# Kernel tuning notes

Hardware: AMD Instinct MI355X
Metric: run time of the kernel (lower is better)

The kernel has to match this reference:

```python
import jax, jax.numpy as jnp
import numpy as np

D_MODEL = 512
N_HEADS = 16
D_HEAD = D_MODEL // N_HEADS


def _relative_shift(pos_score):
    # pos_score: [B, H, T, T]  (Transformer-XL shift trick)
    B, H, T1, T2 = pos_score.shape
    padded = jnp.pad(pos_score, ((0, 0), (0, 0), (0, 0), (1, 0)))  # [B,H,T1,T2+1]
    padded = padded.reshape(B, H, T2 + 1, T1)
    return padded[:, :, 1:].reshape(B, H, T1, T2)


def setup_inputs() -> dict:
    key = jax.random.key(0)
    ks = jax.random.split(key, 12)
    B, T, D = 4, 1024, D_MODEL
    s = 1.0 / np.sqrt(D)
    return {
        "q": jax.random.normal(ks[0], (B, T, D), jnp.float32),
        "k": jax.random.normal(ks[1], (B, T, D), jnp.float32),
        "v": jax.random.normal(ks[2], (B, T, D), jnp.float32),
        "pos_embedding": jax.random.normal(ks[3], (B, T, D), jnp.float32),
        "Wq": jax.random.normal(ks[4], (D, D), jnp.float32) * s,
        "bq": jnp.zeros((D,), jnp.float32),
        "Wp": jax.random.normal(ks[5], (D, D), jnp.float32) * s,
        "Wf": jax.random.normal(ks[6], (D, D), jnp.float32) * s,
        "bf": jnp.zeros((D,), jnp.float32),
        "u_bias": jax.random.normal(ks[7], (N_HEADS, D_HEAD), jnp.float32) * s,
        "v_bias": jax.random.normal(ks[8], (N_HEADS, D_HEAD), jnp.float32) * s,
    }


def reference(q, k, v, pos_embedding, Wq, bq, Wp, Wf, bf, u_bias, v_bias):
    B, T, D = q.shape
    H, Dh = N_HEADS, D_HEAD
    sqrt_dim = jnp.asarray(np.sqrt(D_MODEL), q.dtype)
    # NOTE: original module uses linear_q for q, k AND v (faithful to source)
    qh = (q @ Wq + bq).reshape(B, T, H, Dh)            # [B,T,H,Dh]
    kh = (k @ Wq + bq).reshape(B, T, H, Dh)
    vh = (v @ Wq + bq).reshape(B, T, H, Dh)
    ph = (pos_embedding @ Wp).reshape(B, T, H, Dh)     # no bias

    content_score = jnp.einsum('bthd,bshd->bhts', qh + u_bias, kh)
    pos_score = jnp.einsum('bthd,bshd->bhts', qh + v_bias, ph)
    pos_score = _relative_shift(pos_score)

    score = (content_score + pos_score) / sqrt_dim     # [B,H,T,T]
    attn = jax.nn.softmax(score, axis=-1)              # dropout identity in eval
    context = jnp.einsum('bhts,bshd->bthd', attn, vh).reshape(B, T, D)
    return context @ Wf + bf
```

## Files before the change

### kernel.cpp

```cpp
#include <hip/hip_runtime.h>
#include <hip/hip_bf16.h>

typedef __bf16 bf16;
typedef bf16 bf16x8 __attribute__((ext_vector_type(8)));
typedef bf16 bf16x4 __attribute__((ext_vector_type(4)));
typedef float f32x4 __attribute__((ext_vector_type(4)));
typedef _Float16 f16x4 __attribute__((ext_vector_type(4)));

#define SCALE_LOG2 0.06376237f


__global__ __launch_bounds__(256) void prep_kernel(
    const float* __restrict__ Wq, const float* __restrict__ Wp, const float* __restrict__ Wf,
    bf16* __restrict__ WqT, bf16* __restrict__ WpT, bf16* __restrict__ WfT)
{
  const int tid = threadIdx.x;
  __shared__ bf16 t[64][72];
  const int m = blockIdx.x >> 6;
  const int tb = blockIdx.x & 63;
  const int tr = tb >> 3, tc = tb & 7;
  const float* W = (m == 0) ? Wq : (m == 1) ? Wp : Wf;
  bf16*        O = (m == 0) ? WqT : (m == 1) ? WpT : WfT;
  const int r = tid >> 2, cg = tid & 3;
  {
    const float* src = W + (size_t)(tr * 64 + r) * 512 + tc * 64 + cg * 16;
    f32x4 a = *(const f32x4*)src, b2 = *(const f32x4*)(src + 4);
    f32x4 c = *(const f32x4*)(src + 8), d = *(const f32x4*)(src + 12);
    bf16x8 lo, hi;
#pragma unroll
    for (int j = 0; j < 4; j++) { lo[j] = (bf16)a[j]; lo[4 + j] = (bf16)b2[j]; hi[j] = (bf16)c[j]; hi[4 + j] = (bf16)d[j]; }
    *(bf16x8*)(&t[r][cg * 16])     = lo;
    *(bf16x8*)(&t[r][cg * 16 + 8]) = hi;
  }
  __syncthreads();
  bf16x8 o0, o1;
#pragma unroll
  for (int j = 0; j < 8; j++) { o0[j] = t[cg * 16 + j][r]; o1[j] = t[cg * 16 + 8 + j][r]; }
  bf16* dst = O + (size_t)(tc * 64 + r) * 512 + tr * 64 + cg * 16;
  *(bf16x8*)dst = o0;
  *(bf16x8*)(dst + 8) = o1;
}

__global__ __launch_bounds__(256) void proj_gemm(
    const float* __restrict__ q, const float* __restrict__ k, const float* __restrict__ v,
    const float* __restrict__ pos,
    const bf16* __restrict__ WqT, const bf16* __restrict__ WpT, const float* __restrict__ bq,
    bf16* __restrict__ qh, bf16* __restrict__ kh, bf16* __restrict__ vT, bf16* __restrict__ phx)
{
  __shared__ bf16 ABs[2 * 128 * 72];
  bf16* As = ABs;
  bf16* Bs = ABs + 128 * 72;
  bf16* vtile = ABs;
  const int tid = threadIdx.x;
  const int wave = tid >> 6, lane = tid & 63, quad = lane >> 4, ln = lane & 15;
  const int wg = blockIdx.x;
  const int xcd = wg & 7, sidx = wg >> 3;
  const int tn = sidx & 3;
  const int tm = xcd + ((sidx >> 2) << 3);
  const int kind = tm >> 5;
  const int rr0 = (tm & 31) * 128;
  const float* X = (kind == 0) ? q : (kind == 1) ? k : (kind == 2) ? v : pos;
  const bf16* WT = ((kind < 3) ? WqT : WpT) + (size_t)tn * 128 * 512;
  const int qn_ = (wave & 1) * 64;
  const int qr_ = (wave >> 1) * 64;
  const int srow = tid >> 2, scg = tid & 3;

  f32x4 acc[4][4] = {};

  f32x4  xa0[4], xa1[4];
  bf16x8 wr0[2], wr1[2];
  {
    const float* p0 = X + (size_t)(rr0 + srow) * 512 + scg * 16;
    const float* p1 = X + (size_t)(rr0 + srow + 64) * 512 + scg * 16;
#pragma unroll
    for (int u = 0; u < 4; u++) { xa0[u] = *(const f32x4*)(p0 + u * 4); xa1[u] = *(const f32x4*)(p1 + u * 4); }
    const bf16* w0 = WT + (size_t)srow * 512 + scg * 16;
    const bf16* w1 = WT + (size_t)(srow + 64) * 512 + scg * 16;
    wr0[0] = *(const bf16x8*)w0; wr0[1] = *(const bf16x8*)(w0 + 8);
    wr1[0] = *(const bf16x8*)w1; wr1[1] = *(const bf16x8*)(w1 + 8);
  }

  for (int kk = 0; kk < 8; kk++) {
    __syncthreads();
    {
      bf16x8 lo, hi;
#pragma unroll
      for (int j = 0; j < 4; j++) { lo[j] = (bf16)xa0[0][j]; lo[4 + j] = (bf16)xa0[1][j]; hi[j] = (bf16)xa0[2][j]; hi[4 + j] = (bf16)xa0[3][j]; }
      *(bf16x8*)(As + srow * 72 + scg * 16)     = lo;
      *(bf16x8*)(As + srow * 72 + scg * 16 + 8) = hi;
#pragma unroll
      for (int j = 0; j < 4; j++) { lo[j] = (bf16)xa1[0][j]; lo[4 + j] = (bf16)xa1[1][j]; hi[j] = (bf16)xa1[2][j]; hi[4 + j] = (bf16)xa1[3][j]; }
      *(bf16x8*)(As + (srow + 64) * 72 + scg * 16)     = lo;
      *(bf16x8*)(As + (srow + 64) * 72 + scg * 16 + 8) = hi;
      *(bf16x8*)(Bs + srow * 72 + scg * 16)            = wr0[0];
      *(bf16x8*)(Bs + srow * 72 + scg * 16 + 8)        = wr0[1];
      *(bf16x8*)(Bs + (srow + 64) * 72 + scg * 16)     = wr1[0];
      *(bf16x8*)(Bs + (srow + 64) * 72 + scg * 16 + 8) = wr1[1];
    }
    __syncthreads();

    if (kk < 7) {
      const int k0n = (kk + 1) * 64;
      const float* p0 = X + (size_t)(rr0 + srow) * 512 + k0n + scg * 16;
      const float* p1 = X + (size_t)(rr0 + srow + 64) * 512 + k0n + scg * 16;
#pragma unroll
      for (int u = 0; u < 4; u++) { xa0[u] = *(const f32x4*)(p0 + u * 4); xa1[u] = *(const f32x4*)(p1 + u * 4); }
      const bf16* w0 = WT + (size_t)srow * 512 + k0n + scg * 16;
      const bf16* w1 = WT + (size_t)(srow + 64) * 512 + k0n + scg * 16;
      wr0[0] = *(const bf16x8*)w0; wr0[1] = *(const bf16x8*)(w0 + 8);
      wr1[0] = *(const bf16x8*)w1; wr1[1] = *(const bf16x8*)(w1 + 8);
    }

#pragma unroll
    for (int ks = 0; ks < 2; ks++) {
      bf16x8 wf[4], xf[4];
#pragma unroll
      for (int i = 0; i < 4; i++) {
        wf[i] = *(const bf16x8*)(Bs + (qn_ + i * 16 + ln) * 72 + ks * 32 + quad * 8);
        xf[i] = *(const bf16x8*)(As + (qr_ + i * 16 + ln) * 72 + ks * 32 + quad * 8);
      }
#pragma unroll
      for (int i = 0; i < 4; i++)
#pragma unroll
        for (int j = 0; j < 4; j++)
          acc[i][j] = __builtin_amdgcn_mfma_f32_16x16x32_bf16(wf[i], xf[j], acc[i][j], 0, 0, 0);
    }
  }
  __syncthreads();

  if (kind == 2) {
#pragma unroll
    for (int i = 0; i < 4; i++) {
      const int nloc = qn_ + i * 16 + quad * 4;
      f32x4 b4 = *(const f32x4*)(bq + tn * 128 + nloc);
#pragma unroll
      for (int j = 0; j < 4; j++) {
        const int mloc = qr_ + j * 16 + ln;
        bf16x4 pk;
#pragma unroll
        for (int r = 0; r < 4; r++) pk[r] = (bf16)(acc[i][j][r] + b4[r]);
        *(bf16x4*)(vtile + mloc * 132 + nloc) = pk;
      }
    }
    __syncthreads();
    const int n = tid >> 1, mh = (tid & 1) * 64;
    const int bb2 = rr0 >> 10, tt0 = rr0 & 1023;
    bf16* vdst = vT + ((size_t)(bb2 * 16 + tn * 4 + (n >> 5)) * 32 + (n & 31)) * 1024 + tt0 + mh;
#pragma unroll
    for (int c = 0; c < 8; c++) {
      bf16x8 oc;
#pragma unroll
      for (int e = 0; e < 8; e++) oc[e] = vtile[(mh + c * 8 + e) * 132 + n];
      *(bf16x8*)(vdst + c * 8) = oc;
    }
  } else {
#pragma unroll
    for (int i = 0; i < 4; i++) {
      const int nn0 = tn * 128 + qn_ + i * 16 + quad * 4;
      const int dd0 = nn0 & 31, hh = nn0 >> 5;
      f32x4 b4 = {0.f, 0.f, 0.f, 0.f};
      if (kind < 3) b4 = *(const f32x4*)(bq + nn0);
#pragma unroll
      for (int j = 0; j < 4; j++) {
        const int rr = rr0 + qr_ + j * 16 + ln;
        const int bb = rr >> 10, tt = rr & 1023;
        const size_t base = (size_t)(bb * 16 + hh);
        bf16x4 pk;
#pragma unroll
        for (int r = 0; r < 4; r++) pk[r] = (bf16)(acc[i][j][r] + b4[r]);
        if (kind == 0)      *(bf16x4*)(qh + (base * 1024 + tt) * 32 + dd0) = pk;
        else if (kind == 1) *(bf16x4*)(kh + (base * 1024 + tt) * 32 + dd0) = pk;
        else {
          *(bf16x4*)(phx + (base * 2048 + tt) * 32 + dd0) = pk;
          if (tt <= 1021) *(bf16x4*)(phx + (base * 2048 + tt + 1025) * 32 + dd0) = pk;
          if (tt == 1023) {
            bf16x4 zz = {};
            *(bf16x4*)(phx + (base * 2048 + 1024) * 32 + dd0) = zz;
            *(bf16x4*)(phx + (base * 2048 + 2047) * 32 + dd0) = zz;
          }
        }
      }
    }
  }
}

__global__ __launch_bounds__(256, 4) void attn_kernel(
    const bf16* __restrict__ qh, const bf16* __restrict__ kh,
    const bf16* __restrict__ vT, const bf16* __restrict__ phx,
    const float* __restrict__ u_bias, const float* __restrict__ v_bias,
    float* __restrict__ Oa, float* __restrict__ Ob,
    float* __restrict__ la, float* __restrict__ lb)
{
  __shared__ bf16     kst[2][64 * 40];
  __shared__ bf16     phs[2][128 * 40];
  __shared__ bf16     vst[2][32 * 72];
  __shared__ _Float16 fs[4 * 16 * 84];
  __shared__ bf16     pb[4 * 16 * 72];

  const int tid = threadIdx.x;
  const int wave = tid >> 6, lane = tid & 63, quad = lane >> 4, ln = lane & 15;
  const int wg = blockIdx.x;
  const int bh = wg & 63;
  const int rest = wg >> 6;
  const int tq = rest & 15, sc = rest >> 4;
  const int h = bh & 15, b = bh >> 4;
  const int t0 = tq * 64;
  const bf16* qh_h  = qh  + (size_t)bh * 1024 * 32;
  const bf16* kh_h  = kh  + (size_t)bh * 1024 * 32;
  const bf16* vT_h  = vT  + (size_t)bh * 32 * 1024;
  const bf16* phx_h = phx + (size_t)bh * 2048 * 32;

  _Float16* fsw = fs + wave * 16 * 84;
  bf16*     pbw = pb + wave * 16 * 72;

  const int sr4 = tid >> 2, sc4 = tid & 3;
  const int sr8 = tid >> 3, sc8 = tid & 7;

  const int Ab  = quad * 4 + ((15 - ln) & ~3);
  const int msh = ((15 - ln) & 3) * 16;

  bf16x8 qu, qva, qvn;
  {
    const int t = t0 + wave * 16 + ln;
    bf16x8 q0 = *(const bf16x8*)(qh_h + (size_t)t * 32 + quad * 8);
    bf16x8 q1 = *(const bf16x8*)(qh_h + (size_t)(t + 1) * 32 + quad * 8);
    const float* ubp = u_bias + h * 32 + quad * 8;
    const float* vbp = v_bias + h * 32 + quad * 8;
#pragma unroll
    for (int j = 0; j < 8; j++) {
      qu[j]  = (bf16)(((float)q0[j] + ubp[j]) * SCALE_LOG2);
      qva[j] = (bf16)(((float)q0[j] + vbp[j]) * SCALE_LOG2);
      qvn[j] = (bf16)(((float)q1[j] + vbp[j]) * SCALE_LOG2);
    }
  }

  f32x4 O0 = {0.f, 0.f, 0.f, 0.f}, O1 = {0.f, 0.f, 0.f, 0.f};
  float l_lane = 0.0f;
  const f32x4 zf = {0.f, 0.f, 0.f, 0.f};

  const int si0 = sc * 8;

  bf16x8 g0, g1, g2, g3;
  {
    const int s0p = si0 * 64, jbp = s0p - t0 + 960;
    g0 = *(const bf16x8*)(kh_h  + (size_t)(s0p + sr4) * 32 + sc4 * 8);
    g1 = *(const bf16x8*)(phx_h + (size_t)(jbp + sr4) * 32 + sc4 * 8);
    g2 = *(const bf16x8*)(phx_h + (size_t)(jbp + 64 + sr4) * 32 + sc4 * 8);
    g3 = *(const bf16x8*)(vT_h  + (size_t)sr8 * 1024 + s0p + sc8 * 8);
  }

#pragma unroll 2
  for (int si = si0; si < si0 + 8; si++) {
    const int buf = si & 1;
    const int s0 = si * 64;
    const int jbase = s0 - t0 + 960;
    const int jb0 = jbase + (3 - wave) * 16;
    bf16* kc = kst[buf];
    bf16* pc = phs[buf];
    bf16* vc = vst[buf];

    *(bf16x8*)(kc + sr4 * 40 + sc4 * 8)        = g0;
    *(bf16x8*)(pc + sr4 * 40 + sc4 * 8)        = g1;
    *(bf16x8*)(pc + (64 + sr4) * 40 + sc4 * 8) = g2;
    *(bf16x8*)(vc + sr8 * 72 + sc8 * 8)        = g3;

    __syncthreads();

    if (si != si0 + 7) {
      const int s0n = s0 + 64, jbn = jbase + 64;
      g0 = *(const bf16x8*)(kh_h  + (size_t)(s0n + sr4) * 32 + sc4 * 8);
      g1 = *(const bf16x8*)(phx_h + (size_t)(jbn + sr4) * 32 + sc4 * 8);
      g2 = *(const bf16x8*)(phx_h + (size_t)(jbn + 64 + sr4) * 32 + sc4 * 8);
      g3 = *(const bf16x8*)(vT_h  + (size_t)sr8 * 1024 + s0n + sc8 * 8);
    }

#pragma unroll
    for (int i = 0; i < 5; i++) {
      const int row = (3 - wave + i) * 16 + ln;
      bf16x8 pbf = *(const bf16x8*)(pc + row * 40 + quad * 8);
      bf16x8 bsel = (jb0 + i * 16 >= 1024) ? qvn : qva;
      f32x4 f = __builtin_amdgcn_mfma_f32_16x16x32_bf16(pbf, bsel, zf, 0, 0, 0);
      f16x4 fh;
#pragma unroll
      for (int r = 0; r < 4; r++) fh[r] = (_Float16)f[r];
      *(f16x4*)(fsw + ln * 84 + i * 16 + quad * 4) = fh;
    }

    f32x4 c[4];
#pragma unroll
    for (int cs = 0; cs < 4; cs++) {
      bf16x8 kbf = *(const bf16x8*)(kc + (cs * 16 + ln) * 40 + quad * 8);
      c[cs] = __builtin_amdgcn_mfma_f32_16x16x32_bf16(kbf, qu, zf, 0, 0, 0);
    }

    const _Float16* rowp = fsw + ln * 84;
#pragma unroll
    for (int cs = 0; cs < 4; cs++) {
      const uint64_t v0 = *(const uint64_t*)(rowp + cs * 16 + Ab);
      const uint64_t v1 = *(const uint64_t*)(rowp + cs * 16 + Ab + 4);
      union { uint64_t u; f16x4 v; } W;
      W.u = (v0 >> msh) | ((v1 << 1) << (63 - msh));
      bf16x4 pk;
#pragma unroll
      for (int r = 0; r < 4; r++) {
        const float p = __builtin_amdgcn_exp2f(c[cs][r] + (float)W.v[r]);
        l_lane += p;
        pk[r] = (bf16)p;
      }
      *(bf16x4*)(pbw + ln * 72 + cs * 16 + quad * 4) = pk;
    }

#pragma unroll
    for (int kb = 0; kb < 2; kb++) {
      bf16x8 a  = *(const bf16x8*)(pbw + ln * 72 + kb * 32 + quad * 8);
      bf16x8 b0 = *(const bf16x8*)(vc + ln * 72 + kb * 32 + quad * 8);
      bf16x8 b1 = *(const bf16x8*)(vc + (16 + ln) * 72 + kb * 32 + quad * 8);
      O0 = __builtin_amdgcn_mfma_f32_16x16x32_bf16(a, b0, O0, 0, 0, 0);
      O1 = __builtin_amdgcn_mfma_f32_16x16x32_bf16(a, b1, O1, 0, 0, 0);
    }
  }

  l_lane += __shfl_xor(l_lane, 16);
  l_lane += __shfl_xor(l_lane, 32);

  float* Op = sc ? Ob : Oa;
  float* lp = sc ? lb : la;
#pragma unroll
  for (int r = 0; r < 4; r++) {
    const int t = t0 + wave * 16 + quad * 4 + r;
    const size_t o = ((size_t)(b * 1024 + t)) * 512 + h * 32;
    Op[o + ln]      = O0[r];
    Op[o + 16 + ln] = O1[r];
  }
  if (lane < 16) lp[(size_t)bh * 1024 + t0 + wave * 16 + lane] = l_lane;
}

__global__ __launch_bounds__(256) void out_gemm(
    const float* __restrict__ Oa, const float* __restrict__ Ob,
    const float* __restrict__ la, const float* __restrict__ lb,
    const bf16* __restrict__ WfT, const float* __restrict__ bfv,
    float* __restrict__ out)
{
  __shared__ bf16 As[32 * 40];
  __shared__ bf16 Bs[128 * 40];
  __shared__ float linv[16 * 32];
  const int tid = threadIdx.x;
  const int wave = tid >> 6, lane = tid & 63, quad = lane >> 4, ln = lane & 15;
  const int wg = blockIdx.x;
  const int xcd = wg & 7, sidx = wg >> 3;
  const int tn = sidx & 3;
  const int tm = xcd + ((sidx >> 2) << 3);
  const int rr0 = tm * 32;
  const bf16* WT = WfT + (size_t)tn * 128 * 512;
  const int qm = (wave & 1) * 16, qn = (wave >> 1) * 64;
  const int srow = tid >> 2, scg = tid & 3;
  const int srow8 = tid >> 3, scg8 = tid & 7;

  f32x4 a0, c0;
  bf16x8 b0r, b1r;
  {
    a0 = *(const f32x4*)(Oa + (size_t)(rr0 + srow8) * 512 + scg8 * 4);
    c0 = *(const f32x4*)(Ob + (size_t)(rr0 + srow8) * 512 + scg8 * 4);
    b0r = *(const bf16x8*)(WT + (size_t)srow * 512 + scg * 8);
    b1r = *(const bf16x8*)(WT + (size_t)(srow + 64) * 512 + scg * 8);
  }

  for (int e = tid; e < 512; e += 256) {
    const int hh = e >> 5, r = e & 31;
    const int row = rr0 + r;
    const int b_ = row >> 10, t_ = row & 1023;
    const size_t li = ((size_t)(b_ * 16 + hh)) * 1024 + t_;
    linv[e] = 1.0f / (la[li] + lb[li]);
  }

  f32x4 acc[4] = {};
  for (int kk = 0; kk < 16; kk++) {
    __syncthreads();
    {
      const float s = linv[kk * 32 + srow8];
      bf16x4 t4;
#pragma unroll
      for (int j = 0; j < 4; j++) t4[j] = (bf16)((a0[j] + c0[j]) * s);
      *(bf16x4*)(As + srow8 * 40 + scg8 * 4)      = t4;
      *(bf16x8*)(Bs + srow * 40 + scg * 8)        = b0r;
      *(bf16x8*)(Bs + (srow + 64) * 40 + scg * 8) = b1r;
    }
    __syncthreads();

    if (kk < 15) {
      const int k0n = (kk + 1) * 32;
      a0 = *(const f32x4*)(Oa + (size_t)(rr0 + srow8) * 512 + k0n + scg8 * 4);
      c0 = *(const f32x4*)(Ob + (size_t)(rr0 + srow8) * 512 + k0n + scg8 * 4);
      b0r = *(const bf16x8*)(WT + (size_t)srow * 512 + k0n + scg * 8);
      b1r = *(const bf16x8*)(WT + (size_t)(srow + 64) * 512 + k0n + scg * 8);
    }

    bf16x8 af, bfm[4];
    af = *(const bf16x8*)(As + (qm + ln) * 40 + quad * 8);
#pragma unroll
    for (int j = 0; j < 4; j++)
      bfm[j] = *(const bf16x8*)(Bs + (qn + j * 16 + ln) * 40 + quad * 8);
#pragma unroll
    for (int j = 0; j < 4; j++)
      acc[j] = __builtin_amdgcn_mfma_f32_16x16x32_bf16(af, bfm[j], acc[j], 0, 0, 0);
  }

#pragma unroll
  for (int j = 0; j < 4; j++) {
    const int nn = tn * 128 + qn + j * 16 + ln;
    const float bias = bfv[nn];
#pragma unroll
    for (int r = 0; r < 4; r++) {
      const int rr = rr0 + qm + quad * 4 + r;
      out[(size_t)rr * 512 + nn] = acc[j][r] + bias;
    }
  }
}

extern "C" void kernel_launch(void* const* d_in, const int* in_sizes, int n_in,
                              void* d_out, int out_size, void* d_ws, size_t ws_size,
                              hipStream_t stream) {
  const float* q   = (const float*)d_in[0];
  const float* k   = (const float*)d_in[1];
  const float* v   = (const float*)d_in[2];
  const float* pe  = (const float*)d_in[3];
  const float* Wq  = (const float*)d_in[4];
  const float* bq  = (const float*)d_in[5];
  const float* Wp  = (const float*)d_in[6];
  const float* Wf  = (const float*)d_in[7];
  const float* bfv = (const float*)d_in[8];
  const float* ub  = (const float*)d_in[9];
  const float* vb  = (const float*)d_in[10];

  bf16* ws  = (bf16*)d_ws;
  bf16* qh  = ws;
  bf16* kh  = qh + 2097152;
  bf16* vT  = kh + 2097152;
  bf16* phx = vT + 2097152;
  bf16* WqT = phx + 4194304;
  bf16* WpT = WqT + 262144;
  bf16* WfT = WpT + 262144;
  float* Oa = (float*)(WfT + 262144);
  float* Ob = Oa + 2097152;
  float* la = Ob + 2097152;
  float* lb = la + 65536;

  prep_kernel<<<192, 256, 0, stream>>>(Wq, Wp, Wf, WqT, WpT, WfT);
  proj_gemm<<<512, 256, 0, stream>>>(q, k, v, pe, WqT, WpT, bq, qh, kh, vT, phx);
  attn_kernel<<<2048, 256, 0, stream>>>(qh, kh, vT, phx, ub, vb, Oa, Ob, la, lb);
  out_gemm<<<512, 256, 0, stream>>>(Oa, Ob, la, lb, WfT, bfv, (float*)d_out);
}
```

Baseline: 171.0 us.

## Drop split-KV in attention, normalize in-kernel and emit bf16 context

The attention kernel no longer splits the key range into two halves with separate partial outputs. Each workgroup now walks all 16 key tiles, normalizes by the row sum itself, and writes a bf16 context tensor. This removes the fp32 partial O/l writes and their combine-and-normalize step in the output GEMM, which cuts global traffic. In exchange, grid parallelism halves (1024 workgroups), and LDS double buffering is replaced by single buffers with an extra barrier per iteration, which may expose load latency.

Result: faster. 158.9 us (-7.1%).

```diff
diff --git a/kernel.cpp b/kernel.cpp
--- a/kernel.cpp
+++ b/kernel.cpp
@@ -188,12 +188,11 @@
     const bf16* __restrict__ qh, const bf16* __restrict__ kh,
     const bf16* __restrict__ vT, const bf16* __restrict__ phx,
     const float* __restrict__ u_bias, const float* __restrict__ v_bias,
-    float* __restrict__ Oa, float* __restrict__ Ob,
-    float* __restrict__ la, float* __restrict__ lb)
+    bf16* __restrict__ ctx)
 {
-  __shared__ bf16     kst[2][64 * 40];
-  __shared__ bf16     phs[2][128 * 40];
-  __shared__ bf16     vst[2][32 * 72];
+  __shared__ bf16     kst[64 * 40];
+  __shared__ bf16     phs[128 * 40];
+  __shared__ bf16     vst[32 * 72];
   __shared__ _Float16 fs[4 * 16 * 84];
   __shared__ bf16     pb[4 * 16 * 72];
 
@@ -201,8 +200,7 @@
   const int wave = tid >> 6, lane = tid & 63, quad = lane >> 4, ln = lane & 15;
   const int wg = blockIdx.x;
   const int bh = wg & 63;
-  const int rest = wg >> 6;
-  const int tq = rest & 15, sc = rest >> 4;
+  const int tq = wg >> 6;
   const int h = bh & 15, b = bh >> 4;
   const int t0 = tq * 64;
   const bf16* qh_h  = qh  + (size_t)bh * 1024 * 32;
@@ -238,35 +236,30 @@
   float l_lane = 0.0f;
   const f32x4 zf = {0.f, 0.f, 0.f, 0.f};
 
-  const int si0 = sc * 8;
-
   bf16x8 g0, g1, g2, g3;
   {
-    const int s0p = si0 * 64, jbp = s0p - t0 + 960;
-    g0 = *(const bf16x8*)(kh_h  + (size_t)(s0p + sr4) * 32 + sc4 * 8);
+    const int jbp = -t0 + 960;
+    g0 = *(const bf16x8*)(kh_h  + (size_t)sr4 * 32 + sc4 * 8);
     g1 = *(const bf16x8*)(phx_h + (size_t)(jbp + sr4) * 32 + sc4 * 8);
     g2 = *(const bf16x8*)(phx_h + (size_t)(jbp + 64 + sr4) * 32 + sc4 * 8);
-    g3 = *(const bf16x8*)(vT_h  + (size_t)sr8 * 1024 + s0p + sc8 * 8);
-  }
-
-#pragma unroll 2
-  for (int si = si0; si < si0 + 8; si++) {
-    const int buf = si & 1;
+    g3 = *(const bf16x8*)(vT_h  + (size_t)sr8 * 1024 + sc8 * 8);
+  }
+
+  for (int si = 0; si < 16; si++) {
     const int s0 = si * 64;
     const int jbase = s0 - t0 + 960;
     const int jb0 = jbase + (3 - wave) * 16;
-    bf16* kc = kst[buf];
-    bf16* pc = phs[buf];
-    bf16* vc = vst[buf];
-
-    *(bf16x8*)(kc + sr4 * 40 + sc4 * 8)        = g0;
-    *(bf16x8*)(pc + sr4 * 40 + sc4 * 8)        = g1;
-    *(bf16x8*)(pc + (64 + sr4) * 40 + sc4 * 8) = g2;
-    *(bf16x8*)(vc + sr8 * 72 + sc8 * 8)        = g3;
-
-    __syncthreads();
-
-    if (si != si0 + 7) {
+
+    __syncthreads();
+
+    *(bf16x8*)(kst + sr4 * 40 + sc4 * 8)        = g0;
+    *(bf16x8*)(phs + sr4 * 40 + sc4 * 8)        = g1;
+    *(bf16x8*)(phs + (64 + sr4) * 40 + sc4 * 8) = g2;
+    *(bf16x8*)(vst + sr8 * 72 + sc8 * 8)        = g3;
+
+    __syncthreads();
+
+    if (si != 15) {
       const int s0n = s0 + 64, jbn = jbase + 64;
       g0 = *(const bf16x8*)(kh_h  + (size_t)(s0n + sr4) * 32 + sc4 * 8);
       g1 = *(const bf16x8*)(phx_h + (size_t)(jbn + sr4) * 32 + sc4 * 8);
@@ -277,7 +270,7 @@
 #pragma unroll
     for (int i = 0; i < 5; i++) {
       const int row = (3 - wave + i) * 16 + ln;
-      bf16x8 pbf = *(const bf16x8*)(pc + row * 40 + quad * 8);
+      bf16x8 pbf = *(const bf16x8*)(phs + row * 40 + quad * 8);
       bf16x8 bsel = (jb0 + i * 16 >= 1024) ? qvn : qva;
       f32x4 f = __builtin_amdgcn_mfma_f32_16x16x32_bf16(pbf, bsel, zf, 0, 0, 0);
       f16x4 fh;
@@ -289,7 +282,7 @@
     f32x4 c[4];
 #pragma unroll
     for (int cs = 0; cs < 4; cs++) {
-      bf16x8 kbf = *(const bf16x8*)(kc + (cs * 16 + ln) * 40 + quad * 8);
+      bf16x8 kbf = *(const bf16x8*)(kst + (cs * 16 + ln) * 40 + quad * 8);
       c[cs] = __builtin_amdgcn_mfma_f32_16x16x32_bf16(kbf, qu, zf, 0, 0, 0);
     }
 
@@ -313,8 +306,8 @@
 #pragma unroll
     for (int kb = 0; kb < 2; kb++) {
       bf16x8 a  = *(const bf16x8*)(pbw + ln * 72 + kb * 32 + quad * 8);
-      bf16x8 b0 = *(const bf16x8*)(vc + ln * 72 + kb * 32 + quad * 8);
-      bf16x8 b1 = *(const bf16x8*)(vc + (16 + ln) * 72 + kb * 32 + quad * 8);
+      bf16x8 b0 = *(const bf16x8*)(vst + ln * 72 + kb * 32 + quad * 8);
+      bf16x8 b1 = *(const bf16x8*)(vst + (16 + ln) * 72 + kb * 32 + quad * 8);
       O0 = __builtin_amdgcn_mfma_f32_16x16x32_bf16(a, b0, O0, 0, 0, 0);
       O1 = __builtin_amdgcn_mfma_f32_16x16x32_bf16(a, b1, O1, 0, 0, 0);
     }
@@ -322,28 +315,23 @@
 
   l_lane += __shfl_xor(l_lane, 16);
   l_lane += __shfl_xor(l_lane, 32);
-
-  float* Op = sc ? Ob : Oa;
-  float* lp = sc ? lb : la;
 #pragma unroll
   for (int r = 0; r < 4; r++) {
+    const float lr = __shfl(l_lane, quad * 4 + r);
+    const float inv = 1.0f / lr;
     const int t = t0 + wave * 16 + quad * 4 + r;
     const size_t o = ((size_t)(b * 1024 + t)) * 512 + h * 32;
-    Op[o + ln]      = O0[r];
-    Op[o + 16 + ln] = O1[r];
-  }
-  if (lane < 16) lp[(size_t)bh * 1024 + t0 + wave * 16 + lane] = l_lane;
+    ctx[o + ln]      = (bf16)(O0[r] * inv);
+    ctx[o + 16 + ln] = (bf16)(O1[r] * inv);
+  }
 }
 
 __global__ __launch_bounds__(256) void out_gemm(
-    const float* __restrict__ Oa, const float* __restrict__ Ob,
-    const float* __restrict__ la, const float* __restrict__ lb,
-    const bf16* __restrict__ WfT, const float* __restrict__ bfv,
-    float* __restrict__ out)
+    const bf16* __restrict__ ctx, const bf16* __restrict__ WfT,
+    const float* __restrict__ bfv, float* __restrict__ out)
 {
   __shared__ bf16 As[32 * 40];
   __shared__ bf16 Bs[128 * 40];
-  __shared__ float linv[16 * 32];
   const int tid = threadIdx.x;
   const int wave = tid >> 6, lane = tid & 63, quad = lane >> 4, ln = lane & 15;
   const int wg = blockIdx.x;
@@ -356,41 +344,25 @@
   const int srow = tid >> 2, scg = tid & 3;
   const int srow8 = tid >> 3, scg8 = tid & 7;
 
-  f32x4 a0, c0;
+  bf16x4 a4;
   bf16x8 b0r, b1r;
   {
-    a0 = *(const f32x4*)(Oa + (size_t)(rr0 + srow8) * 512 + scg8 * 4);
-    c0 = *(const f32x4*)(Ob + (size_t)(rr0 + srow8) * 512 + scg8 * 4);
+    a4  = *(const bf16x4*)(ctx + (size_t)(rr0 + srow8) * 512 + scg8 * 4);
     b0r = *(const bf16x8*)(WT + (size_t)srow * 512 + scg * 8);
     b1r = *(const bf16x8*)(WT + (size_t)(srow + 64) * 512 + scg * 8);
   }
 
-  for (int e = tid; e < 512; e += 256) {
-    const int hh = e >> 5, r = e & 31;
-    const int row = rr0 + r;
-    const int b_ = row >> 10, t_ = row & 1023;
-    const size_t li = ((size_t)(b_ * 16 + hh)) * 1024 + t_;
-    linv[e] = 1.0f / (la[li] + lb[li]);
-  }
-
   f32x4 acc[4] = {};
   for (int kk = 0; kk < 16; kk++) {
     __syncthreads();
-    {
-      const float s = linv[kk * 32 + srow8];
-      bf16x4 t4;
-#pragma unroll
-      for (int j = 0; j < 4; j++) t4[j] = (bf16)((a0[j] + c0[j]) * s);
-      *(bf16x4*)(As + srow8 * 40 + scg8 * 4)      = t4;
-      *(bf16x8*)(Bs + srow * 40 + scg * 8)        = b0r;
-      *(bf16x8*)(Bs + (srow + 64) * 40 + scg * 8) = b1r;
-    }
+    *(bf16x4*)(As + srow8 * 40 + scg8 * 4)      = a4;
+    *(bf16x8*)(Bs + srow * 40 + scg * 8)        = b0r;
+    *(bf16x8*)(Bs + (srow + 64) * 40 + scg * 8) = b1r;
     __syncthreads();
 
     if (kk < 15) {
       const int k0n = (kk + 1) * 32;
-      a0 = *(const f32x4*)(Oa + (size_t)(rr0 + srow8) * 512 + k0n + scg8 * 4);
-      c0 = *(const f32x4*)(Ob + (size_t)(rr0 + srow8) * 512 + k0n + scg8 * 4);
+      a4  = *(const bf16x4*)(ctx + (size_t)(rr0 + srow8) * 512 + k0n + scg8 * 4);
       b0r = *(const bf16x8*)(WT + (size_t)srow * 512 + k0n + scg * 8);
       b1r = *(const bf16x8*)(WT + (size_t)(srow + 64) * 512 + k0n + scg * 8);
     }
@@ -440,13 +412,10 @@
   bf16* WqT = phx + 4194304;
   bf16* WpT = WqT + 262144;
   bf16* WfT = WpT + 262144;
-  float* Oa = (float*)(WfT + 262144);
-  float* Ob = Oa + 2097152;
-  float* la = Ob + 2097152;
-  float* lb = la + 65536;
+  bf16* ctx = WfT + 262144;
 
   prep_kernel<<<192, 256, 0, stream>>>(Wq, Wp, Wf, WqT, WpT, WfT);
   proj_gemm<<<512, 256, 0, stream>>>(q, k, v, pe, WqT, WpT, bq, qh, kh, vT, phx);
-  attn_kernel<<<2048, 256, 0, stream>>>(qh, kh, vT, phx, ub, vb, Oa, Ob, la, lb);
-  out_gemm<<<512, 256, 0, stream>>>(Oa, Ob, la, lb, WfT, bfv, (float*)d_out);
+  attn_kernel<<<1024, 256, 0, stream>>>(qh, kh, vT, phx, ub, vb, ctx);
+  out_gemm<<<512, 256, 0, stream>>>(ctx, WfT, bfv, (float*)d_out);
 }
```
